# Optimization experiments

Hardware: AMD Instinct MI355X
Metric: run time of the kernel (lower is better)

## Reference

```python
import jax, jax.numpy as jnp
import numpy as np

N_NODES = 50000


def gcn_conv(x, src, dst, W, b):
    """PyG GCNConv: symmetric-normalized aggregation with self-loops.
    out[i] = sum_{j->i} deg^{-1/2}[j] deg^{-1/2}[i] (x_j @ W) + b
    src/dst already include self-loop edges.
    """
    n = x.shape[0]
    ew = jnp.ones(src.shape[0], dtype=x.dtype)
    deg = jax.ops.segment_sum(ew, dst, num_segments=n)  # [N]
    dinv = jnp.where(deg > 0, jax.lax.rsqrt(deg), 0.0).astype(x.dtype)
    norm = dinv[src] * dinv[dst]  # [E+N]
    xw = x @ W  # [N, z] dense transform first (as PyG does)
    msg = xw[src] * norm[:, None]  # gather + scale, [E+N, z]
    out = jax.ops.segment_sum(msg, dst, num_segments=n)  # scatter-add
    return out + b


def prelu(x, a):
    return jnp.where(x > 0, x, a * x)


def setup_inputs() -> dict:
    key = jax.random.key(0)
    k1, k2, k3, k4 = jax.random.split(key, 4)
    in_dim = z_dim = 96
    n_edges = 800000
    x = jax.random.normal(k1, (N_NODES, in_dim), dtype=jnp.float32)
    edge_index = jax.random.randint(k2, (2, n_edges), 0, N_NODES, dtype=jnp.int32)
    # Glorot-style init for GCN weights
    s1 = 1.0 / np.sqrt(in_dim)
    W1 = jax.random.uniform(k3, (in_dim, z_dim), jnp.float32, -s1, s1)
    W2 = jax.random.uniform(k4, (z_dim, z_dim), jnp.float32, -s1, s1)
    b1 = jnp.zeros((z_dim,), jnp.float32)
    b2 = jnp.zeros((z_dim,), jnp.float32)
    prelu_a = jnp.full((z_dim,), 0.25, jnp.float32)  # shared PReLU, per-channel
    return {"x": x, "edge_index": edge_index, "W1": W1, "b1": b1,
            "W2": W2, "b2": b2, "prelu_a": prelu_a}


def reference(x, edge_index, W1, b1, W2, b2, prelu_a):
    n = x.shape[0]
    loop = jnp.arange(n, dtype=edge_index.dtype)
    src = jnp.concatenate([edge_index[0], loop])
    dst = jnp.concatenate([edge_index[1], loop])
    h = prelu(gcn_conv(x, src, dst, W1, b1), prelu_a)
    h = prelu(gcn_conv(h, src, dst, W2, b2), prelu_a)
    return h
```

## Files before the change

### kernel.cpp

```cpp
#include <hip/hip_runtime.h>
#include <hip/hip_fp16.h>

#define D 96
#define D4 24
#define MAXBINS 256

static inline size_t alignup(size_t x) { return (x + 255) & ~size_t(255); }

__device__ inline float4 f4fma(float s, float4 a, float4 acc) {
    acc.x = fmaf(s, a.x, acc.x);
    acc.y = fmaf(s, a.y, acc.y);
    acc.z = fmaf(s, a.z, acc.z);
    acc.w = fmaf(s, a.w, acc.w);
    return acc;
}

__device__ inline float4 h4fma(const uint2* __restrict__ XH, int s, int t, float w, float4 acc) {
    uint2 rv = XH[(size_t)s * D4 + t];
    __half2 ha = *reinterpret_cast<__half2*>(&rv.x);
    __half2 hb = *reinterpret_cast<__half2*>(&rv.y);
    float2 f0 = __half22float2(ha);
    float2 f1 = __half22float2(hb);
    acc.x = fmaf(w, f0.x, acc.x);
    acc.y = fmaf(w, f0.y, acc.y);
    acc.z = fmaf(w, f1.x, acc.z);
    acc.w = fmaf(w, f1.y, acc.w);
    return acc;
}


__global__ __launch_bounds__(1024) void hist_kernel(const int* __restrict__ dst, int E,
                                                    int* __restrict__ bhist, int nbins) {
    __shared__ int h[MAXBINS];
    const int tid = threadIdx.x;
    if (tid < nbins) h[tid] = 0;
    __syncthreads();
    int e = blockIdx.x * 1024 + tid;
    if (e < E) atomicAdd(&h[dst[e] >> 8], 1);
    __syncthreads();
    if (tid < nbins) bhist[blockIdx.x * nbins + tid] = h[tid];
}

__global__ __launch_bounds__(1024) void scan1_kernel(const int* __restrict__ bhist,
                                                     int* __restrict__ boffs,
                                                     int* __restrict__ bsum,
                                                     int m, int nblk, int nbins) {
    __shared__ int wsum[16];
    const int i = blockIdx.x * 1024 + threadIdx.x;
    const int lane = threadIdx.x & 63;
    const int wid  = threadIdx.x >> 6;
    int v = 0;
    if (i < m) {
        int b = i % nblk, bin = i / nblk;
        v = bhist[b * nbins + bin];
    }
    int sc = v;
    #pragma unroll
    for (int off = 1; off < 64; off <<= 1) {
        int t = __shfl_up(sc, off);
        if (lane >= off) sc += t;
    }
    if (lane == 63) wsum[wid] = sc;
    __syncthreads();
    int wprefix = 0;
    #pragma unroll
    for (int k = 0; k < 16; ++k)
        if (k < wid) wprefix += wsum[k];
    if (i < m) boffs[i] = wprefix + (sc - v);
    if (threadIdx.x == 1023) bsum[blockIdx.x] = wprefix + sc;
}

__global__ __launch_bounds__(1024) void scan2_kernel(const int* __restrict__ bsum,
                                                     int* __restrict__ boff, int nb) {
    __shared__ int wsum[16];
    const int lane = threadIdx.x & 63;
    const int wid  = threadIdx.x >> 6;
    int v = ((int)threadIdx.x < nb) ? bsum[threadIdx.x] : 0;
    int sc = v;
    #pragma unroll
    for (int off = 1; off < 64; off <<= 1) {
        int t = __shfl_up(sc, off);
        if (lane >= off) sc += t;
    }
    if (lane == 63) wsum[wid] = sc;
    __syncthreads();
    int wprefix = 0;
    #pragma unroll
    for (int k = 0; k < 16; ++k)
        if (k < wid) wprefix += wsum[k];
    if ((int)threadIdx.x < nb) boff[threadIdx.x] = wprefix + (sc - v);
}

__global__ __launch_bounds__(1024) void scan3_kernel(int* __restrict__ boffs,
                                                     const int* __restrict__ boff, int m) {
    int i = blockIdx.x * 1024 + threadIdx.x;
    if (i < m) boffs[i] += boff[blockIdx.x];
}

__global__ __launch_bounds__(1024) void dist_kernel(const int* __restrict__ src,
                                                    const int* __restrict__ dst, int E,
                                                    const int* __restrict__ boffs,
                                                    int nblk, int nbins,
                                                    int2* __restrict__ ebuf) {
    __shared__ int h[MAXBINS];
    __shared__ int base[MAXBINS];
    const int tid = threadIdx.x;
    if (tid < nbins) h[tid] = 0;
    __syncthreads();
    int e = blockIdx.x * 1024 + tid;
    int s = 0, d = 0, bin = 0, rank = 0;
    bool valid = e < E;
    if (valid) {
        s = src[e]; d = dst[e];
        bin = d >> 8;
        rank = atomicAdd(&h[bin], 1);
    }
    __syncthreads();
    if (tid < nbins) base[tid] = boffs[tid * nblk + blockIdx.x];
    __syncthreads();
    if (valid) ebuf[base[bin] + rank] = make_int2(s, d);
}

__global__ __launch_bounds__(256) void bucketA_kernel(const int2* __restrict__ ebuf,
                                                      const int* __restrict__ boffs,
                                                      int nblk, int nbins,
                                                      float* __restrict__ dinv,
                                                      int* __restrict__ rowptr,
                                                      int n, int E) {
    __shared__ int cnt[256];
    __shared__ int wsum[4];
    const int k = blockIdx.x;
    const int tid = threadIdx.x;
    const int bstart = boffs[k * nblk];
    const int bend = (k + 1 < nbins) ? boffs[(k + 1) * nblk] : E;
    cnt[tid] = 0;
    __syncthreads();
    for (int e = bstart + tid; e < bend; e += 256)
        atomicAdd(&cnt[ebuf[e].y & 255], 1);
    __syncthreads();
    int v = cnt[tid];
    const int lane = tid & 63, wid = tid >> 6;
    int sc = v;
    #pragma unroll
    for (int off = 1; off < 64; off <<= 1) {
        int t = __shfl_up(sc, off);
        if (lane >= off) sc += t;
    }
    if (lane == 63) wsum[wid] = sc;
    __syncthreads();
    int wprefix = 0;
    #pragma unroll
    for (int w = 0; w < 4; ++w)
        if (w < wid) wprefix += wsum[w];
    int node = k * 256 + tid;
    if (node < n) {
        dinv[node] = rsqrtf((float)(v + 1));
        rowptr[node] = bstart + wprefix + (sc - v);
    }
    if (k == nbins - 1 && tid == 0) rowptr[n] = E;
}

__global__ __launch_bounds__(256) void bucketB_kernel(const int2* __restrict__ ebuf,
                                                      const int* __restrict__ boffs,
                                                      int nblk, int nbins,
                                                      const int* __restrict__ rowptr,
                                                      const float* __restrict__ dinv,
                                                      int2* __restrict__ csr, int E) {
    __shared__ int cnt[256];
    const int k = blockIdx.x;
    const int tid = threadIdx.x;
    const int bstart = boffs[k * nblk];
    const int bend = (k + 1 < nbins) ? boffs[(k + 1) * nblk] : E;
    cnt[tid] = 0;
    __syncthreads();
    for (int e = bstart + tid; e < bend; e += 256) {
        int2 ed = ebuf[e];
        int rank = atomicAdd(&cnt[ed.y & 255], 1);
        csr[rowptr[ed.y] + rank] = make_int2(ed.x, __float_as_int(dinv[ed.x]));
    }
}


__global__ __launch_bounds__(192) void matmul_kernel(const float* __restrict__ X,
                                                     const float* __restrict__ W,
                                                     uint2* __restrict__ Y, int n) {
    __shared__ float XsT[96 * 64];
    const int t = threadIdx.x;
    const int y = threadIdx.y;
    const int tid = y * 24 + t;
    const int row0 = blockIdx.x * 64;
    const float4* X4 = (const float4*)X;

    for (int i = tid; i < 64 * 24; i += 192) {
        int r = i / 24, c4 = i % 24;
        float4 v = make_float4(0.f, 0.f, 0.f, 0.f);
        if (row0 + r < n) v = X4[(size_t)(row0 + r) * D4 + c4];
        int rs = r ^ ((c4 & 15) << 2);
        XsT[(c4 * 4 + 0) * 64 + rs] = v.x;
        XsT[(c4 * 4 + 1) * 64 + rs] = v.y;
        XsT[(c4 * 4 + 2) * 64 + rs] = v.z;
        XsT[(c4 * 4 + 3) * 64 + rs] = v.w;
    }
    __syncthreads();

    const float4* W4 = (const float4*)W;
    float4 acc[8];
    #pragma unroll
    for (int r = 0; r < 8; ++r) acc[r] = make_float4(0.f, 0.f, 0.f, 0.f);
    const int rbase = y * 8;

    #pragma unroll 8
    for (int k = 0; k < 96; ++k) {
        float4 w = W4[k * D4 + t];
        int base0 = (rbase ^ (((k >> 2) & 15) << 2));
        float4 xa = *(const float4*)&XsT[k * 64 + base0];
        float4 xb = *(const float4*)&XsT[k * 64 + (base0 ^ 4)];
        acc[0] = f4fma(xa.x, w, acc[0]);
        acc[1] = f4fma(xa.y, w, acc[1]);
        acc[2] = f4fma(xa.z, w, acc[2]);
        acc[3] = f4fma(xa.w, w, acc[3]);
        acc[4] = f4fma(xb.x, w, acc[4]);
        acc[5] = f4fma(xb.y, w, acc[5]);
        acc[6] = f4fma(xb.z, w, acc[6]);
        acc[7] = f4fma(xb.w, w, acc[7]);
    }

    #pragma unroll
    for (int r = 0; r < 8; ++r) {
        int row = row0 + rbase + r;
        if (row < n) {
            __half2 ha = __float22half2_rn(make_float2(acc[r].x, acc[r].y));
            __half2 hb = __float22half2_rn(make_float2(acc[r].z, acc[r].w));
            uint2 st;
            st.x = *reinterpret_cast<unsigned int*>(&ha);
            st.y = *reinterpret_cast<unsigned int*>(&hb);
            Y[(size_t)row * D4 + t] = st;
        }
    }
}

__global__ __launch_bounds__(384) void aggregate_kernel(const uint2* __restrict__ XH,
                                                        const int2* __restrict__ csr,
                                                        const int* __restrict__ rowptr,
                                                        const float* __restrict__ dinv,
                                                        const float4* __restrict__ b4,
                                                        const float4* __restrict__ pa4,
                                                        float4* __restrict__ out4, int n) {
    const int i = blockIdx.x * 16 + threadIdx.y;
    const int t = threadIdx.x;
    if (i >= n) return;
    const int beg = rowptr[i], end = rowptr[i + 1];
    float4 acc = make_float4(0.f, 0.f, 0.f, 0.f);
    int p = beg;
    for (; p + 8 <= end; p += 8) {
        int2 e0 = csr[p + 0];
        int2 e1 = csr[p + 1];
        int2 e2 = csr[p + 2];
        int2 e3 = csr[p + 3];
        int2 e4 = csr[p + 4];
        int2 e5 = csr[p + 5];
        int2 e6 = csr[p + 6];
        int2 e7 = csr[p + 7];
        acc = h4fma(XH, e0.x, t, __int_as_float(e0.y), acc);
        acc = h4fma(XH, e1.x, t, __int_as_float(e1.y), acc);
        acc = h4fma(XH, e2.x, t, __int_as_float(e2.y), acc);
        acc = h4fma(XH, e3.x, t, __int_as_float(e3.y), acc);
        acc = h4fma(XH, e4.x, t, __int_as_float(e4.y), acc);
        acc = h4fma(XH, e5.x, t, __int_as_float(e5.y), acc);
        acc = h4fma(XH, e6.x, t, __int_as_float(e6.y), acc);
        acc = h4fma(XH, e7.x, t, __int_as_float(e7.y), acc);
    }
    if (p + 4 <= end) {
        int2 e0 = csr[p + 0];
        int2 e1 = csr[p + 1];
        int2 e2 = csr[p + 2];
        int2 e3 = csr[p + 3];
        acc = h4fma(XH, e0.x, t, __int_as_float(e0.y), acc);
        acc = h4fma(XH, e1.x, t, __int_as_float(e1.y), acc);
        acc = h4fma(XH, e2.x, t, __int_as_float(e2.y), acc);
        acc = h4fma(XH, e3.x, t, __int_as_float(e3.y), acc);
        p += 4;
    }
    for (; p < end; ++p) {
        int2 e = csr[p];
        acc = h4fma(XH, e.x, t, __int_as_float(e.y), acc);
    }
    const float di = dinv[i];
    float4 self = make_float4(0.f, 0.f, 0.f, 0.f);
    self = h4fma(XH, i, t, 1.f, self);
    float4 b = b4[t], a = pa4[t];
    float4 v;
    v.x = fmaf(di, acc.x, di * di * self.x) + b.x;
    v.y = fmaf(di, acc.y, di * di * self.y) + b.y;
    v.z = fmaf(di, acc.z, di * di * self.z) + b.z;
    v.w = fmaf(di, acc.w, di * di * self.w) + b.w;
    v.x = v.x > 0.f ? v.x : a.x * v.x;
    v.y = v.y > 0.f ? v.y : a.y * v.y;
    v.z = v.z > 0.f ? v.z : a.z * v.z;
    v.w = v.w > 0.f ? v.w : a.w * v.w;
    out4[(size_t)i * D4 + t] = v;
}

extern "C" void kernel_launch(void* const* d_in, const int* in_sizes, int n_in,
                              void* d_out, int out_size, void* d_ws, size_t ws_size,
                              hipStream_t stream) {
    const float* x   = (const float*)d_in[0];
    const int*   ei  = (const int*)d_in[1];
    const float* W1  = (const float*)d_in[2];
    const float* b1  = (const float*)d_in[3];
    const float* W2  = (const float*)d_in[4];
    const float* b2  = (const float*)d_in[5];
    const float* pa  = (const float*)d_in[6];
    const int n = in_sizes[0] / D;
    const int E = in_sizes[1] / 2;
    const int* srcp = ei;
    const int* dstp = ei + E;

    const int nbins  = (n + 255) / 256;
    const int nblk_e = (E + 1023) / 1024;
    const int m      = nbins * nblk_e;
    const int nbscan = (m + 1023) / 1024;

    char* w = (char*)d_ws;
    int*   bhist  = (int*)w;   w += alignup((size_t)m * 4);
    int*   boffs  = (int*)w;   w += alignup((size_t)m * 4);
    int*   bsum   = (int*)w;   w += alignup(1024 * 4);
    int*   bboff  = (int*)w;   w += alignup(1024 * 4);
    float* dinv   = (float*)w; w += alignup((size_t)n * 4);
    int*   rowptr = (int*)w;   w += alignup((size_t)(n + 1) * 4);
    int2*  ebuf   = (int2*)w;  w += alignup((size_t)E * 8);
    int2*  csr    = (int2*)w;  w += alignup((size_t)E * 8);
    uint2* xw     = (uint2*)w; w += alignup((size_t)n * D * 2);
    float* out    = (float*)d_out;

    hist_kernel<<<nblk_e, 1024, 0, stream>>>(dstp, E, bhist, nbins);
    scan1_kernel<<<nbscan, 1024, 0, stream>>>(bhist, boffs, bsum, m, nblk_e, nbins);
    scan2_kernel<<<1, 1024, 0, stream>>>(bsum, bboff, nbscan);
    scan3_kernel<<<nbscan, 1024, 0, stream>>>(boffs, bboff, m);
    dist_kernel<<<nblk_e, 1024, 0, stream>>>(srcp, dstp, E, boffs, nblk_e, nbins, ebuf);
    bucketA_kernel<<<nbins, 256, 0, stream>>>(ebuf, boffs, nblk_e, nbins, dinv, rowptr, n, E);
    bucketB_kernel<<<nbins, 256, 0, stream>>>(ebuf, boffs, nblk_e, nbins, rowptr, dinv, csr, E);

    dim3 mblk(24, 8);
    const int mgrid = (n + 63) / 64;
    dim3 ablk(24, 16);
    const int agrid = (n + 15) / 16;

    matmul_kernel<<<mgrid, mblk, 0, stream>>>(x, W1, xw, n);
    aggregate_kernel<<<agrid, ablk, 0, stream>>>(xw, csr, rowptr, dinv,
                                                 (const float4*)b1, (const float4*)pa, (float4*)out, n);
    matmul_kernel<<<mgrid, mblk, 0, stream>>>(out, W2, xw, n);
    aggregate_kernel<<<agrid, ablk, 0, stream>>>(xw, csr, rowptr, dinv,
                                                 (const float4*)b2, (const float4*)pa, (float4*)out, n);
}
```

Baseline: 146.0 us.

## Widen aggregate gathers to 16-byte loads and fold scan3 into consumers

The aggregation kernel now uses 12 threads per node, each loading a uint4 holding eight halfs instead of a uint2 holding four. Each block covers 32 nodes so the block still has 384 threads. The separate scan3 kernel is removed; dist and the bucket kernels add the block-level offset themselves when they read boffs. bucketB now seeds per-node cursors from rowptr, so each edge does one shared atomic and skips the rowptr gather. Together these cut launch count and the number of load instructions, at the cost of fewer threads per node and more registers per thread.

```diff
diff --git a/kernel.cpp b/kernel.cpp
--- a/kernel.cpp
+++ b/kernel.cpp
@@ -15,17 +15,23 @@
     return acc;
 }
 
-__device__ inline float4 h4fma(const uint2* __restrict__ XH, int s, int t, float w, float4 acc) {
-    uint2 rv = XH[(size_t)s * D4 + t];
-    __half2 ha = *reinterpret_cast<__half2*>(&rv.x);
-    __half2 hb = *reinterpret_cast<__half2*>(&rv.y);
-    float2 f0 = __half22float2(ha);
-    float2 f1 = __half22float2(hb);
-    acc.x = fmaf(w, f0.x, acc.x);
-    acc.y = fmaf(w, f0.y, acc.y);
-    acc.z = fmaf(w, f1.x, acc.z);
-    acc.w = fmaf(w, f1.y, acc.w);
-    return acc;
+__device__ inline void u4fma(uint4 rv, float w, float4& a0, float4& a1) {
+    __half2 h0 = *reinterpret_cast<__half2*>(&rv.x);
+    __half2 h1 = *reinterpret_cast<__half2*>(&rv.y);
+    __half2 h2 = *reinterpret_cast<__half2*>(&rv.z);
+    __half2 h3 = *reinterpret_cast<__half2*>(&rv.w);
+    float2 f0 = __half22float2(h0);
+    float2 f1 = __half22float2(h1);
+    float2 f2 = __half22float2(h2);
+    float2 f3 = __half22float2(h3);
+    a0.x = fmaf(w, f0.x, a0.x);
+    a0.y = fmaf(w, f0.y, a0.y);
+    a0.z = fmaf(w, f1.x, a0.z);
+    a0.w = fmaf(w, f1.y, a0.w);
+    a1.x = fmaf(w, f2.x, a1.x);
+    a1.y = fmaf(w, f2.y, a1.y);
+    a1.z = fmaf(w, f3.x, a1.z);
+    a1.w = fmaf(w, f3.y, a1.w);
 }
 
 
@@ -91,15 +97,10 @@
     if ((int)threadIdx.x < nb) boff[threadIdx.x] = wprefix + (sc - v);
 }
 
-__global__ __launch_bounds__(1024) void scan3_kernel(int* __restrict__ boffs,
-                                                     const int* __restrict__ boff, int m) {
-    int i = blockIdx.x * 1024 + threadIdx.x;
-    if (i < m) boffs[i] += boff[blockIdx.x];
-}
-
 __global__ __launch_bounds__(1024) void dist_kernel(const int* __restrict__ src,
                                                     const int* __restrict__ dst, int E,
                                                     const int* __restrict__ boffs,
+                                                    const int* __restrict__ bboff,
                                                     int nblk, int nbins,
                                                     int2* __restrict__ ebuf) {
     __shared__ int h[MAXBINS];
@@ -116,13 +117,17 @@
         rank = atomicAdd(&h[bin], 1);
     }
     __syncthreads();
-    if (tid < nbins) base[tid] = boffs[tid * nblk + blockIdx.x];
+    if (tid < nbins) {
+        int idx = tid * nblk + blockIdx.x;
+        base[tid] = boffs[idx] + bboff[idx >> 10];
+    }
     __syncthreads();
     if (valid) ebuf[base[bin] + rank] = make_int2(s, d);
 }
 
 __global__ __launch_bounds__(256) void bucketA_kernel(const int2* __restrict__ ebuf,
                                                       const int* __restrict__ boffs,
+                                                      const int* __restrict__ bboff,
                                                       int nblk, int nbins,
                                                       float* __restrict__ dinv,
                                                       int* __restrict__ rowptr,
@@ -131,8 +136,9 @@
     __shared__ int wsum[4];
     const int k = blockIdx.x;
     const int tid = threadIdx.x;
-    const int bstart = boffs[k * nblk];
-    const int bend = (k + 1 < nbins) ? boffs[(k + 1) * nblk] : E;
+    int i0 = k * nblk, i1 = (k + 1) * nblk;
+    const int bstart = boffs[i0] + bboff[i0 >> 10];
+    const int bend = (k + 1 < nbins) ? (boffs[i1] + bboff[i1 >> 10]) : E;
     cnt[tid] = 0;
     __syncthreads();
     for (int e = bstart + tid; e < bend; e += 256)
@@ -162,21 +168,24 @@
 
 __global__ __launch_bounds__(256) void bucketB_kernel(const int2* __restrict__ ebuf,
                                                       const int* __restrict__ boffs,
+                                                      const int* __restrict__ bboff,
                                                       int nblk, int nbins,
                                                       const int* __restrict__ rowptr,
                                                       const float* __restrict__ dinv,
-                                                      int2* __restrict__ csr, int E) {
-    __shared__ int cnt[256];
+                                                      int2* __restrict__ csr, int n, int E) {
+    __shared__ int cur[256];
     const int k = blockIdx.x;
     const int tid = threadIdx.x;
-    const int bstart = boffs[k * nblk];
-    const int bend = (k + 1 < nbins) ? boffs[(k + 1) * nblk] : E;
-    cnt[tid] = 0;
+    int i0 = k * nblk, i1 = (k + 1) * nblk;
+    const int bstart = boffs[i0] + bboff[i0 >> 10];
+    const int bend = (k + 1 < nbins) ? (boffs[i1] + bboff[i1 >> 10]) : E;
+    int node = k * 256 + tid;
+    cur[tid] = (node < n) ? rowptr[node] : 0;
     __syncthreads();
     for (int e = bstart + tid; e < bend; e += 256) {
         int2 ed = ebuf[e];
-        int rank = atomicAdd(&cnt[ed.y & 255], 1);
-        csr[rowptr[ed.y] + rank] = make_int2(ed.x, __float_as_int(dinv[ed.x]));
+        int pos = atomicAdd(&cur[ed.y & 255], 1);
+        csr[pos] = make_int2(ed.x, __float_as_int(dinv[ed.x]));
     }
 }
 
@@ -239,18 +248,19 @@
     }
 }
 
-__global__ __launch_bounds__(384) void aggregate_kernel(const uint2* __restrict__ XH,
+__global__ __launch_bounds__(384) void aggregate_kernel(const uint4* __restrict__ XH4,
                                                         const int2* __restrict__ csr,
                                                         const int* __restrict__ rowptr,
                                                         const float* __restrict__ dinv,
                                                         const float4* __restrict__ b4,
                                                         const float4* __restrict__ pa4,
                                                         float4* __restrict__ out4, int n) {
-    const int i = blockIdx.x * 16 + threadIdx.y;
+    const int i = blockIdx.x * 32 + threadIdx.y;
     const int t = threadIdx.x;
     if (i >= n) return;
     const int beg = rowptr[i], end = rowptr[i + 1];
-    float4 acc = make_float4(0.f, 0.f, 0.f, 0.f);
+    float4 a0 = make_float4(0.f, 0.f, 0.f, 0.f);
+    float4 a1 = make_float4(0.f, 0.f, 0.f, 0.f);
     int p = beg;
     for (; p + 8 <= end; p += 8) {
         int2 e0 = csr[p + 0];
@@ -261,44 +271,67 @@
         int2 e5 = csr[p + 5];
         int2 e6 = csr[p + 6];
         int2 e7 = csr[p + 7];
-        acc = h4fma(XH, e0.x, t, __int_as_float(e0.y), acc);
-        acc = h4fma(XH, e1.x, t, __int_as_float(e1.y), acc);
-        acc = h4fma(XH, e2.x, t, __int_as_float(e2.y), acc);
-        acc = h4fma(XH, e3.x, t, __int_as_float(e3.y), acc);
-        acc = h4fma(XH, e4.x, t, __int_as_float(e4.y), acc);
-        acc = h4fma(XH, e5.x, t, __int_as_float(e5.y), acc);
-        acc = h4fma(XH, e6.x, t, __int_as_float(e6.y), acc);
-        acc = h4fma(XH, e7.x, t, __int_as_float(e7.y), acc);
+        uint4 r0 = XH4[(size_t)e0.x * 12 + t];
+        uint4 r1 = XH4[(size_t)e1.x * 12 + t];
+        uint4 r2 = XH4[(size_t)e2.x * 12 + t];
+        uint4 r3 = XH4[(size_t)e3.x * 12 + t];
+        uint4 r4 = XH4[(size_t)e4.x * 12 + t];
+        uint4 r5 = XH4[(size_t)e5.x * 12 + t];
+        uint4 r6 = XH4[(size_t)e6.x * 12 + t];
+        uint4 r7 = XH4[(size_t)e7.x * 12 + t];
+        u4fma(r0, __int_as_float(e0.y), a0, a1);
+        u4fma(r1, __int_as_float(e1.y), a0, a1);
+        u4fma(r2, __int_as_float(e2.y), a0, a1);
+        u4fma(r3, __int_as_float(e3.y), a0, a1);
+        u4fma(r4, __int_as_float(e4.y), a0, a1);
+        u4fma(r5, __int_as_float(e5.y), a0, a1);
+        u4fma(r6, __int_as_float(e6.y), a0, a1);
+        u4fma(r7, __int_as_float(e7.y), a0, a1);
     }
     if (p + 4 <= end) {
         int2 e0 = csr[p + 0];
         int2 e1 = csr[p + 1];
         int2 e2 = csr[p + 2];
         int2 e3 = csr[p + 3];
-        acc = h4fma(XH, e0.x, t, __int_as_float(e0.y), acc);
-        acc = h4fma(XH, e1.x, t, __int_as_float(e1.y), acc);
-        acc = h4fma(XH, e2.x, t, __int_as_float(e2.y), acc);
-        acc = h4fma(XH, e3.x, t, __int_as_float(e3.y), acc);
+        uint4 r0 = XH4[(size_t)e0.x * 12 + t];
+        uint4 r1 = XH4[(size_t)e1.x * 12 + t];
+        uint4 r2 = XH4[(size_t)e2.x * 12 + t];
+        uint4 r3 = XH4[(size_t)e3.x * 12 + t];
+        u4fma(r0, __int_as_float(e0.y), a0, a1);
+        u4fma(r1, __int_as_float(e1.y), a0, a1);
+        u4fma(r2, __int_as_float(e2.y), a0, a1);
+        u4fma(r3, __int_as_float(e3.y), a0, a1);
         p += 4;
     }
     for (; p < end; ++p) {
         int2 e = csr[p];
-        acc = h4fma(XH, e.x, t, __int_as_float(e.y), acc);
+        u4fma(XH4[(size_t)e.x * 12 + t], __int_as_float(e.y), a0, a1);
     }
     const float di = dinv[i];
-    float4 self = make_float4(0.f, 0.f, 0.f, 0.f);
-    self = h4fma(XH, i, t, 1.f, self);
-    float4 b = b4[t], a = pa4[t];
-    float4 v;
-    v.x = fmaf(di, acc.x, di * di * self.x) + b.x;
-    v.y = fmaf(di, acc.y, di * di * self.y) + b.y;
-    v.z = fmaf(di, acc.z, di * di * self.z) + b.z;
-    v.w = fmaf(di, acc.w, di * di * self.w) + b.w;
-    v.x = v.x > 0.f ? v.x : a.x * v.x;
-    v.y = v.y > 0.f ? v.y : a.y * v.y;
-    v.z = v.z > 0.f ? v.z : a.z * v.z;
-    v.w = v.w > 0.f ? v.w : a.w * v.w;
-    out4[(size_t)i * D4 + t] = v;
+    float4 s0 = make_float4(0.f, 0.f, 0.f, 0.f);
+    float4 s1 = make_float4(0.f, 0.f, 0.f, 0.f);
+    u4fma(XH4[(size_t)i * 12 + t], 1.f, s0, s1);
+    float4 b0 = b4[2 * t], b1 = b4[2 * t + 1];
+    float4 q0 = pa4[2 * t], q1 = pa4[2 * t + 1];
+    float4 v0, v1;
+    v0.x = fmaf(di, a0.x, di * di * s0.x) + b0.x;
+    v0.y = fmaf(di, a0.y, di * di * s0.y) + b0.y;
+    v0.z = fmaf(di, a0.z, di * di * s0.z) + b0.z;
+    v0.w = fmaf(di, a0.w, di * di * s0.w) + b0.w;
+    v1.x = fmaf(di, a1.x, di * di * s1.x) + b1.x;
+    v1.y = fmaf(di, a1.y, di * di * s1.y) + b1.y;
+    v1.z = fmaf(di, a1.z, di * di * s1.z) + b1.z;
+    v1.w = fmaf(di, a1.w, di * di * s1.w) + b1.w;
+    v0.x = v0.x > 0.f ? v0.x : q0.x * v0.x;
+    v0.y = v0.y > 0.f ? v0.y : q0.y * v0.y;
+    v0.z = v0.z > 0.f ? v0.z : q0.z * v0.z;
+    v0.w = v0.w > 0.f ? v0.w : q0.w * v0.w;
+    v1.x = v1.x > 0.f ? v1.x : q1.x * v1.x;
+    v1.y = v1.y > 0.f ? v1.y : q1.y * v1.y;
+    v1.z = v1.z > 0.f ? v1.z : q1.z * v1.z;
+    v1.w = v1.w > 0.f ? v1.w : q1.w * v1.w;
+    out4[(size_t)i * D4 + 2 * t] = v0;
+    out4[(size_t)i * D4 + 2 * t + 1] = v1;
 }
 
 extern "C" void kernel_launch(void* const* d_in, const int* in_sizes, int n_in,
@@ -330,26 +363,27 @@
     int*   rowptr = (int*)w;   w += alignup((size_t)(n + 1) * 4);
     int2*  ebuf   = (int2*)w;  w += alignup((size_t)E * 8);
     int2*  csr    = (int2*)w;  w += alignup((size_t)E * 8);
-    uint2* xw     = (uint2*)w; w += alignup((size_t)n * D * 2);
+    uint4* xw     = (uint4*)w; w += alignup((size_t)n * D * 2);
     float* out    = (float*)d_out;
 
     hist_kernel<<<nblk_e, 1024, 0, stream>>>(dstp, E, bhist, nbins);
     scan1_kernel<<<nbscan, 1024, 0, stream>>>(bhist, boffs, bsum, m, nblk_e, nbins);
     scan2_kernel<<<1, 1024, 0, stream>>>(bsum, bboff, nbscan);
-    scan3_kernel<<<nbscan, 1024, 0, stream>>>(boffs, bboff, m);
-    dist_kernel<<<nblk_e, 1024, 0, stream>>>(srcp, dstp, E, boffs, nblk_e, nbins, ebuf);
-    bucketA_kernel<<<nbins, 256, 0, stream>>>(ebuf, boffs, nblk_e, nbins, dinv, rowptr, n, E);
-    bucketB_kernel<<<nbins, 256, 0, stream>>>(ebuf, boffs, nblk_e, nbins, rowptr, dinv, csr, E);
+    dist_kernel<<<nblk_e, 1024, 0, stream>>>(srcp, dstp, E, boffs, bboff, nblk_e, nbins, ebuf);
+    bucketA_kernel<<<nbins, 256, 0, stream>>>(ebuf, boffs, bboff, nblk_e, nbins,
+                                              dinv, rowptr, n, E);
+    bucketB_kernel<<<nbins, 256, 0, stream>>>(ebuf, boffs, bboff, nblk_e, nbins,
+                                              rowptr, dinv, csr, n, E);
 
     dim3 mblk(24, 8);
     const int mgrid = (n + 63) / 64;
-    dim3 ablk(24, 16);
-    const int agrid = (n + 15) / 16;
-
-    matmul_kernel<<<mgrid, mblk, 0, stream>>>(x, W1, xw, n);
+    dim3 ablk(12, 32);
+    const int agrid = (n + 31) / 32;
+
+    matmul_kernel<<<mgrid, mblk, 0, stream>>>(x, W1, (uint2*)xw, n);
     aggregate_kernel<<<agrid, ablk, 0, stream>>>(xw, csr, rowptr, dinv,
                                                  (const float4*)b1, (const float4*)pa, (float4*)out, n);
-    matmul_kernel<<<mgrid, mblk, 0, stream>>>(out, W2, xw, n);
+    matmul_kernel<<<mgrid, mblk, 0, stream>>>(out, W2, (uint2*)xw, n);
     aggregate_kernel<<<agrid, ablk, 0, stream>>>(xw, csr, rowptr, dinv,
                                                  (const float4*)b2, (const float4*)pa, (float4*)out, n);
 }
```

Result: no change. 148.4 us (+1.6%).
